# Kernel tuning notes

Hardware: AMD Instinct MI355X
Metric: run time of the kernel (lower is better)

The kernel has to match this reference:

```python
import jax, jax.numpy as jnp
import numpy as np
from jax import lax

B, N, AH, AW = 32, 128, 512, 512
IMG_H = IMG_W = 2048


def setup_inputs() -> dict:
    key = jax.random.key(0)
    k1, k2, k3, k4, k5, k6 = jax.random.split(key, 6)
    # sigmoid-like attention probabilities in (0,1)
    att = jax.random.uniform(k1, (B, 1, AH, AW), jnp.float32, 1e-4, 1.0 - 1e-4)
    x1 = jax.random.uniform(k2, (B, N), jnp.float32, 0.0, IMG_W * 0.7)
    y1 = jax.random.uniform(k3, (B, N), jnp.float32, 0.0, IMG_H * 0.7)
    bw = jax.random.uniform(k4, (B, N), jnp.float32, 8.0, IMG_W * 0.25)
    bh = jax.random.uniform(k5, (B, N), jnp.float32, 8.0, IMG_H * 0.25)
    x2 = jnp.minimum(x1 + bw, float(IMG_W))
    y2 = jnp.minimum(y1 + bh, float(IMG_H))
    lab = jnp.where(jax.random.uniform(k6, (B, N)) < 0.85, 0.0, -1.0)
    bboxs = jnp.stack([x1, y1, x2, y2, lab], axis=-1)
    return {"attention_mask": att, "bboxs": bboxs, "img_h": IMG_H, "img_w": IMG_W}


def reference(attention_mask, bboxs, img_h, img_w):
    Bn, _, Ah, Aw = attention_mask.shape
    f32 = attention_mask.dtype
    sx = Aw / img_w
    sy = Ah / img_h
    labels = bboxs[:, :, 4]
    c = bboxs[:, :, :4]
    # validity: label != -1 and all coords within image (torch filters sequentially == AND)
    valid = (labels != -1.0) & (c[:, :, 0] <= img_w) & (c[:, :, 1] <= img_h) \
            & (c[:, :, 2] <= img_w) & (c[:, :, 3] <= img_h)
    scaled = c * jnp.array([sx, sy, sx, sy], dtype=f32)  # [B,N,4] in attention coords
    xs = jnp.arange(Aw)
    ys = jnp.arange(Ah)

    def per_image(att, boxes, vmask):
        def step(mask, bv):
            box, v = bv
            bx1, by1, bx2, by2 = box[0], box[1], box[2], box[3]
            fx1 = jnp.floor(bx1); fy1 = jnp.floor(by1)
            x1m = fx1 + 1.0 - bx1; y1m = fy1 + 1.0 - by1          # anti-alias edge margins
            x2m = bx2 - jnp.floor(bx2); y2m = by2 - jnp.floor(by2)
            x1 = jnp.maximum(fx1, 0.0).astype(jnp.int32)
            y1 = jnp.maximum(fy1, 0.0).astype(jnp.int32)
            x2 = jnp.minimum(jnp.ceil(bx2) + 1.0, Aw).astype(jnp.int32)
            y2 = jnp.minimum(jnp.ceil(by2) + 1.0, Ah).astype(jnp.int32)
            one = jnp.ones((), f32)
            colw = jnp.where(xs == x1, x1m, one) * jnp.where(xs == x2 - 1, x2m, one)
            roww = jnp.where(ys == y1, y1m, one) * jnp.where(ys == y2 - 1, y2m, one)
            inb = (((ys >= y1) & (ys < y2))[:, None]) & (((xs >= x1) & (xs < x2))[None, :])
            val = roww[:, None] * colw[None, :]
            # later boxes overwrite earlier ones inside their region (matches torch slice-assign)
            mask = jnp.where(v & inb, val, mask)
            return mask, None

        mask_gt, _ = lax.scan(step, jnp.zeros((Ah, Aw), f32), (boxes, vmask))
        p = att[0]
        # BCE with torch-style log clamping at -100
        log_p = jnp.maximum(jnp.log(p), -100.0)
        log_1mp = jnp.maximum(jnp.log1p(-p), -100.0)
        bce = -jnp.mean(mask_gt * log_p + (1.0 - mask_gt) * log_1mp)
        return jnp.where(jnp.any(vmask), bce, jnp.zeros((), f32))

    losses = jax.vmap(per_image)(attention_mask, scaled, valid)
    return jnp.mean(losses, axis=0, keepdims=True)
```

## Files before the change

### kernel.cpp

```cpp
#include <hip/hip_runtime.h>
#include <hip/hip_bf16.h>

#define B_   32
#define N_   128
#define AH_  512
#define AW_  512
#define LCAP 64
#define LN2  0.69314718055994530942f

#define CFENCE() asm volatile("" ::: "memory")

typedef __fp16 h2_t __attribute__((ext_vector_type(2)));
union f_h2 { float f; h2_t h; };

__global__ __launch_bounds__(128) void row_bce_kernel(
    const float* __restrict__ att,
    const float* __restrict__ bboxs,
    const int*   __restrict__ img_h_p,
    const int*   __restrict__ img_w_p,
    float*       __restrict__ wave_sums)
{
    const int t    = threadIdx.x;
    const int lane = t & 63;
    const int wid  = t >> 6;
    const int task = (blockIdx.x << 1) | wid;
    const int b    = task >> 8;
    const int y0   = (task & 255) << 1;

    __shared__ float4 s_geo[2][LCAP];
    __shared__ float  s_mask[2][2][AW_];

    const float4* p4 = (const float4*)(att + ((size_t)b * AH_ + y0) * AW_);
    float4 P[2][2];
    #pragma unroll
    for (int r = 0; r < 2; ++r)
        #pragma unroll
        for (int h = 0; h < 2; ++h)
            P[r][h] = p4[r * 128 + h * 64 + lane];

    const float fw  = (float)(*img_w_p);
    const float fh  = (float)(*img_h_p);
    const float sxs = (float)AW_ / fw;
    const float sys = (float)AH_ / fh;

    bool   act_any[2];
    float4 rec[2];
    #pragma unroll
    for (int k = 0; k < 2; ++k) {
        const int n = lane + 64 * k;
        const float* bp = bboxs + ((size_t)b * N_ + n) * 5;
        const float c0 = bp[0], c1 = bp[1], c2 = bp[2], c3 = bp[3], lab = bp[4];
        const bool valid = (lab != -1.0f) && (c0 <= fw) && (c1 <= fh)
                                          && (c2 <= fw) && (c3 <= fh);
        const float bx1 = c0 * sxs, by1 = c1 * sys;
        const float bx2 = c2 * sxs, by2 = c3 * sys;
        const float fx1 = floorf(bx1), fy1 = floorf(by1);
        const float x1m = fx1 + 1.0f - bx1;
        const float y1m = fy1 + 1.0f - by1;
        const float x2m = bx2 - floorf(bx2);
        const float y2m = by2 - floorf(by2);
        const int x1 = (int)fmaxf(fx1, 0.0f);
        const int y1 = (int)fmaxf(fy1, 0.0f);
        const int x2 = (int)fminf(ceilf(bx2) + 1.0f, (float)AW_);
        const int y2 = (int)fminf(ceilf(by2) + 1.0f, (float)AH_);

        int   ab = 0;
        float rv0 = 1.0f, rv1 = 1.0f;
        #pragma unroll
        for (int r = 0; r < 2; ++r) {
            const int y = y0 + r;
            const bool a = valid && (y >= y1) && (y < y2);
            ab |= a ? (1 << r) : 0;
            const float rw = ((y == y1)     ? y1m : 1.0f)
                           * ((y == y2 - 1) ? y2m : 1.0f);
            if (r == 0) rv0 = rw; else rv1 = rw;
        }
        act_any[k] = (ab != 0) && (x1 < x2);

        f_h2 u;
        u.h = __builtin_amdgcn_cvt_pkrtz(x1m, x2m);
        rec[k] = make_float4(
            __int_as_float((unsigned)x1 | ((unsigned)x2 << 10) | ((unsigned)ab << 20)),
            u.f, rv0, rv1);
    }

    const unsigned long long ltm  = (1ull << lane) - 1ull;
    const unsigned long long bal0 = __ballot(act_any[0]);
    const unsigned long long bal1 = __ballot(act_any[1]);
    const bool have = (bal0 | bal1) != 0ull;

    float* m0 = s_mask[wid][0];
    float* m1 = s_mask[wid][1];
    float4* mrow4 = (float4*)m0;

    if (have) {
        const float4 z = make_float4(0.f, 0.f, 0.f, 0.f);
        #pragma unroll
        for (int q = 0; q < 4; ++q) mrow4[lane + 64 * q] = z;
        CFENCE();

        #pragma unroll
        for (int k = 0; k < 2; ++k) {
            const unsigned long long bal = (k == 0) ? bal0 : bal1;
            const int cnt = __popcll(bal);
            if (cnt == 0) continue;
            if (act_any[k]) {
                const int slot = __popcll(bal & ltm);
                s_geo[wid][slot] = rec[k];
            }
            CFENCE();

            float4 gA = s_geo[wid][0];
            float4 gB = (cnt > 1) ? s_geo[wid][1] : gA;
            for (int j = 0; j < cnt; ++j) {
                const float4 g = gA;
                gA = gB;
                if (j + 2 < cnt) gB = s_geo[wid][j + 2];

                const int px = __builtin_amdgcn_readfirstlane(__float_as_int(g.x));
                const int e1 = px & 1023;
                const int e2 = (px >> 10) & 1023;
                const int ab = px >> 20;
                f_h2 u; u.f = g.y;
                const float x1m = (float)u.h.x;
                const float x2m = (float)u.h.y;

                const int iters = (e2 - e1 + 63) >> 6;
                for (int q = 0; q < iters; ++q) {
                    const int xr = e1 + (q << 6) + lane;
                    const int x  = (xr < e2) ? xr : (e2 - 1);
                    const float edge = ((x == e1)     ? x1m : 1.0f)
                                     * ((x == e2 - 1) ? x2m : 1.0f);
                    if (ab & 1) m0[x] = g.z * edge;
                    if (ab & 2) m1[x] = g.w * edge;
                }
            }
            CFENCE();
        }
    }

    float acc = 0.0f;
    #pragma unroll
    for (int r = 0; r < 2; ++r) {
        #pragma unroll
        for (int h = 0; h < 2; ++h) {
            const float4 p = P[r][h];
            float4 m = make_float4(0.f, 0.f, 0.f, 0.f);
            if (have) m = mrow4[r * 128 + h * 64 + lane];
            const float pv[4] = {p.x, p.y, p.z, p.w};
            const float mv[4] = {m.x, m.y, m.z, m.w};
            #pragma unroll
            for (int j = 0; j < 4; ++j) {
                const float lp = __log2f(pv[j]);
                const float l1 = __log2f(1.0f - pv[j]);
                acc += l1 + mv[j] * (lp - l1);
            }
        }
    }
    acc *= LN2;

    #pragma unroll
    for (int off = 32; off; off >>= 1) acc += __shfl_down(acc, off, 64);
    if (lane == 0) wave_sums[task] = acc;
}

__global__ __launch_bounds__(1024) void final_kernel(
    const float* __restrict__ bboxs,
    const int*   __restrict__ img_h_p,
    const int*   __restrict__ img_w_p,
    const float* __restrict__ wave_sums,
    float*       __restrict__ out)
{
    const int t = threadIdx.x;
    const int b = t >> 5;
    const int j = t & 31;

    __shared__ float s_loss[B_];

    float s = 0.0f;
    #pragma unroll
    for (int k = 0; k < 8; ++k) s += wave_sums[b * 256 + j + 32 * k];

    const float fw = (float)(*img_w_p);
    const float fh = (float)(*img_h_p);
    int av = 0;
    const float* bp = bboxs + (size_t)b * N_ * 5;
    #pragma unroll
    for (int n = j * 4; n < j * 4 + 4; ++n) {
        const float c0 = bp[n * 5 + 0];
        const float c1 = bp[n * 5 + 1];
        const float c2 = bp[n * 5 + 2];
        const float c3 = bp[n * 5 + 3];
        const float lab = bp[n * 5 + 4];
        av |= ((lab != -1.0f) && (c0 <= fw) && (c1 <= fh)
                              && (c2 <= fw) && (c3 <= fh)) ? 1 : 0;
    }

    #pragma unroll
    for (int off = 16; off; off >>= 1) {
        s  += __shfl_down(s, off, 64);
        av |= __shfl_down(av, off, 64);
    }
    if (j == 0) s_loss[b] = av ? (-s * (1.0f / (float)(AH_ * AW_))) : 0.0f;
    __syncthreads();

    if (t < 64) {
        float v = (t < B_) ? s_loss[t] : 0.0f;
        #pragma unroll
        for (int off = 32; off; off >>= 1) v += __shfl_down(v, off, 64);
        if (t == 0) out[0] = v * (1.0f / (float)B_);
    }
}

extern "C" void kernel_launch(void* const* d_in, const int* in_sizes, int n_in,
                              void* d_out, int out_size, void* d_ws, size_t ws_size,
                              hipStream_t stream)
{
    const float* att   = (const float*)d_in[0];
    const float* bboxs = (const float*)d_in[1];
    const int*   img_h = (const int*)d_in[2];
    const int*   img_w = (const int*)d_in[3];
    float* out = (float*)d_out;
    float* wave_sums = (float*)d_ws;

    row_bce_kernel<<<B_ * AH_ / 4, 128, 0, stream>>>(att, bboxs, img_h, img_w, wave_sums);
    final_kernel<<<1, 1024, 0, stream>>>(bboxs, img_h, img_w, wave_sums, out);
}
```

Before: 29.89 us.

## Process eight rows per wave to amortize box setup and painting

Each wave now handles eight attention rows instead of two. The per-box geometry decode, ballot and compaction are shared across more rows, and each painted column is written to up to eight shared-memory rows, with a fast path for boxes that cover all eight. This reduces redundant box processing and the number of partial sums. In exchange it raises register use (16 float4 prefetches per lane) and shared memory per block, and cuts the grid to a quarter of its former size, which may lower occupancy and latency hiding.

```diff
diff --git a/kernel.cpp b/kernel.cpp
--- a/kernel.cpp
+++ b/kernel.cpp
@@ -24,16 +24,16 @@
     const int lane = t & 63;
     const int wid  = t >> 6;
     const int task = (blockIdx.x << 1) | wid;
-    const int b    = task >> 8;
-    const int y0   = (task & 255) << 1;
+    const int b    = task >> 6;
+    const int y0   = (task & 63) << 3;
 
     __shared__ float4 s_geo[2][LCAP];
-    __shared__ float  s_mask[2][2][AW_];
+    __shared__ float  s_mask[2][8][AW_];
 
     const float4* p4 = (const float4*)(att + ((size_t)b * AH_ + y0) * AW_);
-    float4 P[2][2];
-    #pragma unroll
-    for (int r = 0; r < 2; ++r)
+    float4 P[8][2];
+    #pragma unroll
+    for (int r = 0; r < 8; ++r)
         #pragma unroll
         for (int h = 0; h < 2; ++h)
             P[r][h] = p4[r * 128 + h * 64 + lane];
@@ -64,24 +64,23 @@
         const int x2 = (int)fminf(ceilf(bx2) + 1.0f, (float)AW_);
         const int y2 = (int)fminf(ceilf(by2) + 1.0f, (float)AH_);
 
-        int   ab = 0;
-        float rv0 = 1.0f, rv1 = 1.0f;
-        #pragma unroll
-        for (int r = 0; r < 2; ++r) {
-            const int y = y0 + r;
-            const bool a = valid && (y >= y1) && (y < y2);
-            ab |= a ? (1 << r) : 0;
-            const float rw = ((y == y1)     ? y1m : 1.0f)
-                           * ((y == y2 - 1) ? y2m : 1.0f);
-            if (r == 0) rv0 = rw; else rv1 = rw;
-        }
-        act_any[k] = (ab != 0) && (x1 < x2);
+        const int lo = (y1 > y0) ? (y1 - y0) : 0;
+        const int hi = ((y2 - 1) < (y0 + 7)) ? (y2 - 1 - y0) : 7;
+        const bool any = valid && (lo <= hi) && (y2 > y0) && (y1 < y0 + 8)
+                               && (x1 < x2);
+        int ab = 0;
+        if (any) ab = ((0xFF >> (7 - hi)) & (0xFF << lo)) & 0xFF;
+        act_any[k] = any && (ab != 0);
+
+        const int yA = y0 + lo, yB = y0 + hi;
+        const float rvA = ((yA == y1) ? y1m : 1.0f) * ((yA == y2 - 1) ? y2m : 1.0f);
+        const float rvB = ((yB == y1) ? y1m : 1.0f) * ((yB == y2 - 1) ? y2m : 1.0f);
 
         f_h2 u;
         u.h = __builtin_amdgcn_cvt_pkrtz(x1m, x2m);
         rec[k] = make_float4(
             __int_as_float((unsigned)x1 | ((unsigned)x2 << 10) | ((unsigned)ab << 20)),
-            u.f, rv0, rv1);
+            u.f, rvA, rvB);
     }
 
     const unsigned long long ltm  = (1ull << lane) - 1ull;
@@ -89,14 +88,15 @@
     const unsigned long long bal1 = __ballot(act_any[1]);
     const bool have = (bal0 | bal1) != 0ull;
 
-    float* m0 = s_mask[wid][0];
-    float* m1 = s_mask[wid][1];
-    float4* mrow4 = (float4*)m0;
+    float* m[8];
+    #pragma unroll
+    for (int r = 0; r < 8; ++r) m[r] = s_mask[wid][r];
+    float4* mrow4 = (float4*)m[0];
 
     if (have) {
         const float4 z = make_float4(0.f, 0.f, 0.f, 0.f);
         #pragma unroll
-        for (int q = 0; q < 4; ++q) mrow4[lane + 64 * q] = z;
+        for (int q = 0; q < 16; ++q) mrow4[lane + 64 * q] = z;
         CFENCE();
 
         #pragma unroll
@@ -110,29 +110,55 @@
             }
             CFENCE();
 
-            float4 gA = s_geo[wid][0];
-            float4 gB = (cnt > 1) ? s_geo[wid][1] : gA;
+            float4 g_cur = s_geo[wid][0];
             for (int j = 0; j < cnt; ++j) {
-                const float4 g = gA;
-                gA = gB;
-                if (j + 2 < cnt) gB = s_geo[wid][j + 2];
-
-                const int px = __builtin_amdgcn_readfirstlane(__float_as_int(g.x));
-                const int e1 = px & 1023;
-                const int e2 = (px >> 10) & 1023;
-                const int ab = px >> 20;
+                const float4 g = g_cur;
+                if (j + 1 < cnt) g_cur = s_geo[wid][j + 1];
+
+                const unsigned pks =
+                    (unsigned)__builtin_amdgcn_readfirstlane(__float_as_int(g.x));
+                const int e1 = (int)(pks & 1023u);
+                const int e2 = (int)((pks >> 10) & 1023u);
+                const int ab = (int)(pks >> 20);
+                const int r1 = __builtin_ctz(ab);
+                const int r2 = 31 - __builtin_clz(ab);
                 f_h2 u; u.f = g.y;
                 const float x1m = (float)u.h.x;
                 const float x2m = (float)u.h.y;
+                const float v1  = g.z;
+                const float v2  = g.w;
 
                 const int iters = (e2 - e1 + 63) >> 6;
-                for (int q = 0; q < iters; ++q) {
-                    const int xr = e1 + (q << 6) + lane;
-                    const int x  = (xr < e2) ? xr : (e2 - 1);
-                    const float edge = ((x == e1)     ? x1m : 1.0f)
-                                     * ((x == e2 - 1) ? x2m : 1.0f);
-                    if (ab & 1) m0[x] = g.z * edge;
-                    if (ab & 2) m1[x] = g.w * edge;
+                if (ab == 255) {
+                    for (int q = 0; q < iters; ++q) {
+                        const int xr = e1 + (q << 6) + lane;
+                        const int x  = (xr < e2) ? xr : (e2 - 1);
+                        const float edge = ((x == e1)     ? x1m : 1.0f)
+                                         * ((x == e2 - 1) ? x2m : 1.0f);
+                        const float a1 = v1 * edge;
+                        const float a2 = v2 * edge;
+                        m[0][x] = a1;
+                        m[1][x] = edge; m[2][x] = edge; m[3][x] = edge;
+                        m[4][x] = edge; m[5][x] = edge; m[6][x] = edge;
+                        m[7][x] = a2;
+                    }
+                } else {
+                    for (int q = 0; q < iters; ++q) {
+                        const int xr = e1 + (q << 6) + lane;
+                        const int x  = (xr < e2) ? xr : (e2 - 1);
+                        const float edge = ((x == e1)     ? x1m : 1.0f)
+                                         * ((x == e2 - 1) ? x2m : 1.0f);
+                        const float a1 = v1 * edge;
+                        const float a2 = v2 * edge;
+                        #pragma unroll
+                        for (int r = 0; r < 8; ++r) {
+                            if (ab & (1 << r)) {
+                                const float val = (r == r1) ? a1
+                                                : ((r == r2) ? a2 : edge);
+                                m[r][x] = val;
+                            }
+                        }
+                    }
                 }
             }
             CFENCE();
@@ -141,14 +167,14 @@
 
     float acc = 0.0f;
     #pragma unroll
-    for (int r = 0; r < 2; ++r) {
+    for (int r = 0; r < 8; ++r) {
         #pragma unroll
         for (int h = 0; h < 2; ++h) {
             const float4 p = P[r][h];
-            float4 m = make_float4(0.f, 0.f, 0.f, 0.f);
-            if (have) m = mrow4[r * 128 + h * 64 + lane];
+            float4 mm = make_float4(0.f, 0.f, 0.f, 0.f);
+            if (have) mm = mrow4[r * 128 + h * 64 + lane];
             const float pv[4] = {p.x, p.y, p.z, p.w};
-            const float mv[4] = {m.x, m.y, m.z, m.w};
+            const float mv[4] = {mm.x, mm.y, mm.z, mm.w};
             #pragma unroll
             for (int j = 0; j < 4; ++j) {
                 const float lp = __log2f(pv[j]);
@@ -179,7 +205,7 @@
 
     float s = 0.0f;
     #pragma unroll
-    for (int k = 0; k < 8; ++k) s += wave_sums[b * 256 + j + 32 * k];
+    for (int k = 0; k < 2; ++k) s += wave_sums[b * 64 + j + 32 * k];
 
     const float fw = (float)(*img_w_p);
     const float fh = (float)(*img_h_p);
@@ -223,6 +249,6 @@
     float* out = (float*)d_out;
     float* wave_sums = (float*)d_ws;
 
-    row_bce_kernel<<<B_ * AH_ / 4, 128, 0, stream>>>(att, bboxs, img_h, img_w, wave_sums);
+    row_bce_kernel<<<B_ * AH_ / 16, 128, 0, stream>>>(att, bboxs, img_h, img_w, wave_sums);
     final_kernel<<<1, 1024, 0, stream>>>(bboxs, img_h, img_w, wave_sums, out);
 }
```

New measurement: 25.78 us. 13.8% less time.
